# Kernel optimization log

Measured on AMD Instinct MI355X. Metric: run time of the kernel, lower is better.

Reference implementation:

```python
import jax, jax.numpy as jnp
import numpy as np

B, L, V, E, D, NH, HD, NL = 4, 2048, 32000, 300, 128, 4, 128, 3
D2 = NH * HD  # 512
W = 3  # ring window size (unfold_size)
EPS = 1e-5


def setup_inputs() -> dict:
    key = jax.random.key(0)
    ks = jax.random.split(key, 16)
    s = 0.02
    w = lambda k, shape: (jax.random.normal(k, shape, jnp.float32) * s)
    inp = {
        "tokens": jax.random.randint(ks[0], (B, L), 0, V),
        "mask": jax.random.randint(ks[1], (B, L), 0, 2).astype(jnp.int32),
        "emb_table": w(ks[2], (V, E)),
        "proj_w": w(ks[3], (D, E)),
        "proj_b": jnp.zeros((D,), jnp.float32),
        "ng": jnp.ones((NL, D), jnp.float32),
        "nb": jnp.zeros((NL, D), jnp.float32),
        "rq_w": w(ks[4], (NL, D2, D)), "rq_b": jnp.zeros((NL, D2), jnp.float32),
        "rk_w": w(ks[5], (NL, D2, D)), "rk_b": jnp.zeros((NL, D2), jnp.float32),
        "rv_w": w(ks[6], (NL, D2, D)), "rv_b": jnp.zeros((NL, D2), jnp.float32),
        "ro_w": w(ks[7], (NL, D, D2)), "ro_b": jnp.zeros((NL, D), jnp.float32),
        "sq_w": w(ks[8], (NL, D2, D)), "sq_b": jnp.zeros((NL, D2), jnp.float32),
        "sk_w": w(ks[9], (NL, D2, D)), "sk_b": jnp.zeros((NL, D2), jnp.float32),
        "sv_w": w(ks[10], (NL, D2, D)), "sv_b": jnp.zeros((NL, D2), jnp.float32),
        "so_w": w(ks[11], (NL, D, D2)), "so_b": jnp.zeros((NL, D), jnp.float32),
    }
    return inp


def _layernorm(x, g, b):
    mu = x.mean(-1, keepdims=True)
    var = x.var(-1, keepdims=True)
    return (x - mu) / jnp.sqrt(var + EPS) * g + b


def reference(tokens, mask, emb_table, proj_w, proj_b, ng, nb,
              rq_w, rq_b, rk_w, rk_b, rv_w, rv_b, ro_w, ro_b,
              sq_w, sq_b, sk_w, sk_b, sv_w, sv_b, so_w, so_b):
    b, l = tokens.shape
    pad = (mask == 0)                                        # [B,L] True at padding
    smask = jnp.concatenate([jnp.zeros((b, 1), bool), pad], axis=1)  # [B,L+1]
    x = emb_table[tokens] @ proj_w.T + proj_b                # [B,L,D]
    nodes = x
    relay = x.mean(axis=1)                                   # [B,D]
    r_embs = x                                               # fixed original embeddings
    scale = 1.0 / np.sqrt(HD).astype(np.float32)
    for i in range(NL):
        nx = _layernorm(nodes, ng[i], nb[i])
        # ----- MSA1: ring (windowed) attention + relay extras -----
        q = (nx @ rq_w[i].T + rq_b[i]).reshape(b, l, NH, HD)
        k = (nx @ rk_w[i].T + rk_b[i]).reshape(b, l, NH, HD)
        v = (nx @ rv_w[i].T + rv_b[i]).reshape(b, l, NH, HD)
        relay_bc = jnp.broadcast_to(relay[:, None, :], (b, l, D))
        ax = jnp.stack([r_embs, relay_bc], axis=2)           # [B,L,2,D]
        ak = (ax @ rk_w[i].T + rk_b[i]).reshape(b, l, 2, NH, HD)
        av = (ax @ rv_w[i].T + rv_b[i]).reshape(b, l, 2, NH, HD)
        kp = jnp.pad(k, ((0, 0), (1, 1), (0, 0), (0, 0)))    # zero pad like F.unfold
        vp = jnp.pad(v, ((0, 0), (1, 1), (0, 0), (0, 0)))
        kw = jnp.stack([kp[:, u:u + l] for u in range(W)], axis=2)  # [B,L,3,NH,HD]
        vw = jnp.stack([vp[:, u:u + l] for u in range(W)], axis=2)
        kall = jnp.concatenate([kw, ak], axis=2)             # [B,L,5,NH,HD]
        vall = jnp.concatenate([vw, av], axis=2)
        scores = jnp.einsum('blnh,blunh->blun', q, kall) * scale
        alphas = jax.nn.softmax(scores, axis=2)
        att = jnp.einsum('blun,blunh->blnh', alphas, vall).reshape(b, l, D2)
        nodes = nodes + jax.nn.leaky_relu(att @ ro_w[i].T + ro_b[i])
        # ----- MSA2: relay (global) attention over [relay; nodes] -----
        y = jnp.concatenate([relay[:, None, :], nodes], axis=1)      # [B,L+1,D]
        sq = (relay @ sq_w[i].T + sq_b[i]).reshape(b, NH, HD)
        sk = (y @ sk_w[i].T + sk_b[i]).reshape(b, l + 1, NH, HD)
        sv = (y @ sv_w[i].T + sv_b[i]).reshape(b, l + 1, NH, HD)
        pre = jnp.einsum('bnh,blnh->bnl', sq, sk) * scale            # [B,NH,L+1]
        pre = jnp.where(smask[:, None, :], -jnp.inf, pre)
        al = jax.nn.softmax(pre, axis=2)
        satt = jnp.einsum('bnl,blnh->bnh', al, sv).reshape(b, D2)
        relay = jax.nn.leaky_relu(satt @ so_w[i].T + so_b[i])
        nodes = jnp.where(pad[:, :, None], 0.0, nodes)
    return relay  # a_v: [B, d_model] (use_attention=False path)
```

## Files before the change

kernel.cpp:

```cpp
#include <hip/hip_runtime.h>
#include <hip/hip_bf16.h>

constexpr int B = 4, L = 2048, E = 300, D = 128, NH = 4, HD = 128, NL = 3, D2 = 512;
constexpr float EPS = 1e-5f;
constexpr float SCALE = 0.08838834764831843f;
constexpr int NCH = 64;

typedef unsigned int uint_t;
typedef unsigned short u16;
typedef short bf16x8 __attribute__((ext_vector_type(8)));
typedef float f32x4 __attribute__((ext_vector_type(4)));

__device__ __forceinline__ u16 f2bf(float f) {
  union { float f; uint_t i; } x; x.f = f;
  uint_t r = x.i + 0x7fffu + ((x.i >> 16) & 1u);
  return (u16)(r >> 16);
}
__device__ __forceinline__ uint_t packbf(float a, float b) {
  return (uint_t)f2bf(a) | ((uint_t)f2bf(b) << 16);
}
__device__ __forceinline__ float bf2f(u16 u) {
  union { uint_t i; float f; } x; x.i = ((uint_t)u) << 16; return x.f;
}
__device__ __forceinline__ float2 bf2x2(uint_t u) {
  union { uint_t i; float f; } a, b;
  a.i = (u & 0xffffu) << 16; b.i = u & 0xffff0000u;
  return make_float2(a.f, b.f);
}
struct f8 { float v[8]; };
__device__ __forceinline__ f8 unpack8(uint4 u) {
  f8 r;
  float2 a = bf2x2(u.x); r.v[0] = a.x; r.v[1] = a.y;
  float2 b = bf2x2(u.y); r.v[2] = b.x; r.v[3] = b.y;
  float2 c = bf2x2(u.z); r.v[4] = c.x; r.v[5] = c.y;
  float2 d = bf2x2(u.w); r.v[6] = d.x; r.v[7] = d.y;
  return r;
}

struct WCArgs { const float* s[4]; u16* d[4]; };
__global__ __launch_bounds__(256) void wconv(WCArgs wa) {
  int ti = blockIdx.y;
  const float* s = wa.s[ti]; u16* dd = wa.d[ti];
  int i = (blockIdx.x * 256 + threadIdx.x) * 4;
  float4 f = *(const float4*)(s + i);
  *(uint2*)(dd + i) = make_uint2(packbf(f.x, f.y), packbf(f.z, f.w));
}

struct GDesc { const u16* A; const u16* W; const float* bias; u16* outb; };
struct GArgs { GDesc d[5]; };
struct PArgs {
  const float* rel;
  const float* rkw; const float* rkb;
  const float* rvw; const float* rvb;
  const float* sqw; const float* sqb;
  const float* skw; const float* skb;
  float* relay_k; float* relay_v;
  float* u; float* cvec;
};
constexpr int NPROJ = 24;

__global__ __launch_bounds__(256) void gemm_qkv(GArgs ga, PArgs pa, int N) {
  int bid = blockIdx.x;
  int t = threadIdx.x;
  if (bid < NPROJ) {
    __shared__ float rel[D];
    __shared__ float sql2[2][HD];
    __shared__ float credp[4];
    int b = bid / 6, j = bid % 6;
    if (t < D) rel[t] = pa.rel[(size_t)b * D + t];
    __syncthreads();
    const float4* r4 = (const float4*)rel;
    if (j < 4) {
      int which = j >> 1;
      int n = (j & 1) * 256 + t;
      const float* W = which ? pa.rvw : pa.rkw;
      float acc = (which ? pa.rvb : pa.rkb)[n];
      const float4* w4 = (const float4*)(W + (size_t)n * D);
#pragma unroll 8
      for (int i = 0; i < D / 4; i++) {
        float4 w = w4[i], r = r4[i];
        acc += w.x * r.x + w.y * r.y + w.z * r.z + w.w * r.w;
      }
      (which ? pa.relay_v : pa.relay_k)[(size_t)b * D2 + n] = acc;
    } else {
      int hh = t >> 7, th = t & 127;
      int n = (j - 4) * 2 + hh;
      int nh = n * HD + th;
      float acc = pa.sqb[nh];
      const float4* w4 = (const float4*)(pa.sqw + (size_t)nh * D);
#pragma unroll 8
      for (int i = 0; i < D / 4; i++) {
        float4 w = w4[i], r = r4[i];
        acc += w.x * r.x + w.y * r.y + w.z * r.z + w.w * r.w;
      }
      sql2[hh][th] = acc;
      __syncthreads();
      float cp = acc * pa.skb[nh];
#pragma unroll
      for (int o = 1; o < 64; o <<= 1) cp += __shfl_xor(cp, o, 64);
      if ((t & 63) == 0) credp[t >> 6] = cp;
      float a0 = 0.f, a1 = 0.f, a2 = 0.f, a3 = 0.f;
      const float* wp = pa.skw + (size_t)(n * HD) * D + th;
      for (int hx = 0; hx < HD; hx += 4) {
        a0 += sql2[hh][hx] * wp[(size_t)hx * D];
        a1 += sql2[hh][hx + 1] * wp[(size_t)(hx + 1) * D];
        a2 += sql2[hh][hx + 2] * wp[(size_t)(hx + 2) * D];
        a3 += sql2[hh][hx + 3] * wp[(size_t)(hx + 3) * D];
      }
      pa.u[((size_t)b * NH + n) * D + th] = (a0 + a1 + a2 + a3) * SCALE;
      __syncthreads();
      if (th == 0) pa.cvec[b * NH + n] = (credp[2 * hh] + credp[2 * hh + 1]) * SCALE;
    }
    return;
  }
  __shared__ u16 As[128][136];
  __shared__ u16 Ws[128][136];
  int g = bid - NPROJ;
  int bm = g & 63;
  int y = g >> 6;
  int di = y >> 2, bn = y & 3;
  GDesc d = ga.d[di];
  const int rowA = bm * 128, rowW = bn * 128;

  f32x4 acc[4][4];
#pragma unroll
  for (int i = 0; i < 4; i++)
#pragma unroll
    for (int j = 0; j < 4; j++)
      acc[i][j] = (f32x4){0.f, 0.f, 0.f, 0.f};

  const int r = t >> 1, c0 = (t & 1) * 64;
  const int wid = t >> 6;
  const int wm = (wid & 1) * 64, wn = (wid >> 1) * 64;
  const int lr = t & 15, quad = (t >> 4) & 3;

  const u16* Arow = d.A + (size_t)(rowA + r) * 128;
  const u16* Wrow = d.W + (size_t)(rowW + r) * 128;
  uint4 av_[8], wv_[8];
#pragma unroll
  for (int i = 0; i < 8; i++) {
    av_[i] = *(const uint4*)(Arow + c0 + i * 8);
    wv_[i] = *(const uint4*)(Wrow + c0 + i * 8);
  }
#pragma unroll
  for (int i = 0; i < 8; i++) {
    *(uint4*)&As[r][c0 + i * 8] = av_[i];
    *(uint4*)&Ws[r][c0 + i * 8] = wv_[i];
  }
  __syncthreads();
#pragma unroll
  for (int ks = 0; ks < 4; ks++) {
    bf16x8 af[4], bfr[4];
#pragma unroll
    for (int mt = 0; mt < 4; mt++)
      af[mt] = *(const bf16x8*)&As[wm + mt * 16 + lr][ks * 32 + quad * 8];
#pragma unroll
    for (int nt = 0; nt < 4; nt++)
      bfr[nt] = *(const bf16x8*)&Ws[wn + nt * 16 + lr][ks * 32 + quad * 8];
#pragma unroll
    for (int mt = 0; mt < 4; mt++)
#pragma unroll
      for (int nt = 0; nt < 4; nt++)
        acc[mt][nt] = __builtin_amdgcn_mfma_f32_16x16x32_bf16(af[mt], bfr[nt], acc[mt][nt], 0, 0, 0);
  }
  __syncthreads();
#pragma unroll
  for (int nt = 0; nt < 4; nt++) {
    int colL = wn + nt * 16 + lr;
    float bv = d.bias[rowW + colL];
#pragma unroll
    for (int mt = 0; mt < 4; mt++) {
#pragma unroll
      for (int rr = 0; rr < 4; rr++) {
        int rowL = wm + mt * 16 + quad * 4 + rr;
        As[rowL][colL] = f2bf(acc[mt][nt][rr] + bv);
      }
    }
  }
  __syncthreads();
#pragma unroll
  for (int rep = 0; rep < 8; rep++) {
    int lin = rep * 256 + t;
    int rowL = lin >> 4, colL = (lin & 15) * 8;
    uint4 v = *(const uint4*)&As[rowL][colL];
    *(uint4*)&d.outb[(size_t)(rowA + rowL) * N + rowW + colL] = v;
  }
}

__global__ __launch_bounds__(256) void gemm_embed_ln(
    const float* __restrict__ emb, const float* __restrict__ W,
    const float* __restrict__ bias, const int* __restrict__ gather,
    const float* __restrict__ lng, const float* __restrict__ lnb,
    float* __restrict__ nodes, u16* __restrict__ xb, u16* __restrict__ nxb,
    float* __restrict__ relay) {
  __shared__ u16 As[64][72];
  __shared__ u16 Ws[128][72];
  __shared__ float C[64][132];
  __shared__ float gb[2][D];
  __shared__ float lmu[64], lrs[64];
  int t = threadIdx.x;
  int bm = blockIdx.x;
  const int rowA0 = bm * 64;

  f32x4 acc[2][4];
#pragma unroll
  for (int i = 0; i < 2; i++)
#pragma unroll
    for (int j = 0; j < 4; j++)
      acc[i][j] = (f32x4){0.f, 0.f, 0.f, 0.f};

  const int wid = t >> 6;
  const int wm = (wid & 1) * 32, wn = (wid >> 1) * 64;
  const int lr = t & 15, quad = (t >> 4) & 3;
  const int ra = t >> 2, ca = (t & 3) * 16;
  const int rw = t >> 1, cw = (t & 1) * 32;

  if (t < D) { gb[0][t] = lng[t]; gb[1][t] = lnb[t]; }

  const float* Arow = emb + (size_t)gather[rowA0 + ra] * E;
  const float* Wrow = W + (size_t)rw * E;

  for (int kt = 0; kt < E; kt += 64) {
    __syncthreads();
    bool full = (kt + 64 <= E);
#pragma unroll
    for (int ch = 0; ch < 4; ch++) {
      int c = kt + ca + ch * 4;
      float4 fa;
      if (full) fa = *(const float4*)(Arow + c);
      else {
        fa.x = (c + 0 < E) ? Arow[c + 0] : 0.f;
        fa.y = (c + 1 < E) ? Arow[c + 1] : 0.f;
        fa.z = (c + 2 < E) ? Arow[c + 2] : 0.f;
        fa.w = (c + 3 < E) ? Arow[c + 3] : 0.f;
      }
      *(uint2*)&As[ra][ca + ch * 4] = make_uint2(packbf(fa.x, fa.y), packbf(fa.z, fa.w));
    }
#pragma unroll
    for (int ch = 0; ch < 8; ch++) {
      int c = kt + cw + ch * 4;
      float4 fw;
      if (full) fw = *(const float4*)(Wrow + c);
      else {
        fw.x = (c + 0 < E) ? Wrow[c + 0] : 0.f;
        fw.y = (c + 1 < E) ? Wrow[c + 1] : 0.f;
        fw.z = (c + 2 < E) ? Wrow[c + 2] : 0.f;
        fw.w = (c + 3 < E) ? Wrow[c + 3] : 0.f;
      }
      *(uint2*)&Ws[rw][cw + ch * 4] = make_uint2(packbf(fw.x, fw.y), packbf(fw.z, fw.w));
    }
    __syncthreads();
#pragma unroll
    for (int ks = 0; ks < 2; ks++) {
      bf16x8 af[2], bfr[4];
#pragma unroll
      for (int mt = 0; mt < 2; mt++)
        af[mt] = *(const bf16x8*)&As[wm + mt * 16 + lr][ks * 32 + quad * 8];
#pragma unroll
      for (int nt = 0; nt < 4; nt++)
        bfr[nt] = *(const bf16x8*)&Ws[wn + nt * 16 + lr][ks * 32 + quad * 8];
#pragma unroll
      for (int mt = 0; mt < 2; mt++)
#pragma unroll
        for (int nt = 0; nt < 4; nt++)
          acc[mt][nt] = __builtin_amdgcn_mfma_f32_16x16x32_bf16(af[mt], bfr[nt], acc[mt][nt], 0, 0, 0);
    }
  }
#pragma unroll
  for (int nt = 0; nt < 4; nt++) {
    int col = wn + nt * 16 + lr;
    float bv = bias[col];
#pragma unroll
    for (int mt = 0; mt < 2; mt++) {
#pragma unroll
      for (int rr = 0; rr < 4; rr++) {
        int row = wm + mt * 16 + quad * 4 + rr;
        C[row][col] = acc[mt][nt][rr] + bv;
      }
    }
  }
  __syncthreads();
  if (t < 64) {
    float s = 0.f, s2 = 0.f;
#pragma unroll 16
    for (int j = 0; j < D; j++) { float v = C[t][j]; s += v; s2 += v * v; }
    float mu = s * (1.0f / D);
    float var = s2 * (1.0f / D) - mu * mu;
    lmu[t] = mu; lrs[t] = rsqrtf(var + EPS);
  }
  __syncthreads();
#pragma unroll
  for (int rep = 0; rep < 8; rep++) {
    int lin = rep * 1024 + t * 4;
    int row = lin >> 7, col = lin & 127;
    float4 v = *(const float4*)&C[row][col];
    size_t g = (size_t)(rowA0 + row) * D + col;
    *(float4*)&nodes[g] = v;
    *(uint2*)&xb[g] = make_uint2(packbf(v.x, v.y), packbf(v.z, v.w));
    float mu = lmu[row], rs = lrs[row];
    float o0 = (v.x - mu) * rs * gb[0][col] + gb[1][col];
    float o1 = (v.y - mu) * rs * gb[0][col + 1] + gb[1][col + 1];
    float o2 = (v.z - mu) * rs * gb[0][col + 2] + gb[1][col + 2];
    float o3 = (v.w - mu) * rs * gb[0][col + 3] + gb[1][col + 3];
    *(uint2*)&nxb[g] = make_uint2(packbf(o0, o1), packbf(o2, o3));
  }
  if (t < D) {
    int b = rowA0 >> 11;
    float s = 0.f;
#pragma unroll 16
    for (int r2 = 0; r2 < 64; r2++) s += C[r2][t];
    atomicAdd(&relay[b * D + t], s * (1.0f / L));
  }
}

__global__ __launch_bounds__(256) void gemm_ro_ln(
    const u16* __restrict__ A,
    const u16* __restrict__ W,
    const float* __restrict__ bias,
    const int* __restrict__ mask,
    const float* __restrict__ lng, const float* __restrict__ lnb,
    const float* __restrict__ uvec, const float* __restrict__ cvec,
    float* __restrict__ nodes, u16* __restrict__ nxb,
    float* __restrict__ pm, float* __restrict__ ps, float* __restrict__ pw,
    int do_ln) {
  __shared__ u16 As[32][136];
  __shared__ u16 Ws[128][136];
  __shared__ float C[32][132];
  __shared__ float gb[2][D];
  __shared__ float lmu[32], lrs[32];
  __shared__ float usv[NH][D];
  __shared__ float cv2[NH];
  __shared__ float scs[NH][32];
  __shared__ float esr[NH][32];
  int t = threadIdx.x;
  int bm = blockIdx.x;
  const int rowA0 = bm * 32;
  const int b4 = rowA0 >> 11;
  const int chunk = (rowA0 >> 5) & 63;

  f32x4 acc[4];
#pragma unroll
  for (int j = 0; j < 4; j++) acc[j] = (f32x4){0.f, 0.f, 0.f, 0.f};

  const int wid = t >> 6;
  const int wm = (wid & 1) * 16, wn = (wid >> 1) * 64;
  const int lr = t & 15, quad = (t >> 4) & 3;
  const int ra = t >> 3, ca = (t & 7) * 16;
  const int rw = t >> 1, cw = (t & 1) * 64;

  if (do_ln && t < D) { gb[0][t] = lng[t]; gb[1][t] = lnb[t]; }
#pragma unroll
  for (int rep = 0; rep < 2; rep++) {
    int idx = rep * 256 + t;
    usv[idx >> 7][idx & 127] = uvec[(size_t)b4 * NH * D + idx];
  }
  if (t < NH) cv2[t] = cvec[b4 * NH + t];

  const u16* Arow = A + (size_t)(rowA0 + ra) * 512;
  const u16* Wrow = W + (size_t)rw * 512;

  for (int kt = 0; kt < 512; kt += 128) {
    uint4 a0 = *(const uint4*)(Arow + kt + ca);
    uint4 a1 = *(const uint4*)(Arow + kt + ca + 8);
    uint4 w0 = *(const uint4*)(Wrow + kt + cw);
    uint4 w1 = *(const uint4*)(Wrow + kt + cw + 8);
    uint4 w2 = *(const uint4*)(Wrow + kt + cw + 16);
    uint4 w3 = *(const uint4*)(Wrow + kt + cw + 24);
    uint4 w4 = *(const uint4*)(Wrow + kt + cw + 32);
    uint4 w5 = *(const uint4*)(Wrow + kt + cw + 40);
    uint4 w6 = *(const uint4*)(Wrow + kt + cw + 48);
    uint4 w7 = *(const uint4*)(Wrow + kt + cw + 56);
    __syncthreads();
    *(uint4*)&As[ra][ca] = a0; *(uint4*)&As[ra][ca + 8] = a1;
    *(uint4*)&Ws[rw][cw] = w0; *(uint4*)&Ws[rw][cw + 8] = w1;
    *(uint4*)&Ws[rw][cw + 16] = w2; *(uint4*)&Ws[rw][cw + 24] = w3;
    *(uint4*)&Ws[rw][cw + 32] = w4; *(uint4*)&Ws[rw][cw + 40] = w5;
    *(uint4*)&Ws[rw][cw + 48] = w6; *(uint4*)&Ws[rw][cw + 56] = w7;
    __syncthreads();
#pragma unroll
    for (int ks = 0; ks < 4; ks++) {
      bf16x8 af = *(const bf16x8*)&As[wm + lr][ks * 32 + quad * 8];
      bf16x8 bfr[4];
#pragma unroll
      for (int nt = 0; nt < 4; nt++)
        bfr[nt] = *(const bf16x8*)&Ws[wn + nt * 16 + lr][ks * 32 + quad * 8];
#pragma unroll
      for (int nt = 0; nt < 4; nt++)
        acc[nt] = __builtin_amdgcn_mfma_f32_16x16x32_bf16(af, bfr[nt], acc[nt], 0, 0, 0);
    }
  }
  __syncthreads();
#pragma unroll
  for (int nt = 0; nt < 4; nt++) {
    int col = wn + nt * 16 + lr;
    float bv = bias[col];
#pragma unroll
    for (int rr = 0; rr < 4; rr++) {
      int row = wm + quad * 4 + rr;
      float v = acc[nt][rr] + bv;
      v = (v > 0.f) ? v : 0.01f * v;
      v += nodes[(size_t)(rowA0 + row) * D + col];
      if (mask[rowA0 + row] == 0) v = 0.f;
      C[row][col] = v;
    }
  }
  __syncthreads();
  if (t < 32) {
    float s = 0.f, s2 = 0.f;
#pragma unroll 16
    for (int j = 0; j < D; j++) { float v = C[t][j]; s += v; s2 += v * v; }
    float mu = s * (1.0f / D);
    float var = s2 * (1.0f / D) - mu * mu;
    lmu[t] = mu; lrs[t] = rsqrtf(var + EPS);
  }
  __syncthreads();
#pragma unroll
  for (int rep = 0; rep < 4; rep++) {
    int lin = rep * 1024 + t * 4;
    int row = lin >> 7, col = lin & 127;
    float4 v = *(const float4*)&C[row][col];
    size_t g = (size_t)(rowA0 + row) * D + col;
    *(float4*)&nodes[g] = v;
    if (do_ln) {
      float mu = lmu[row], rs = lrs[row];
      float o0 = (v.x - mu) * rs * gb[0][col] + gb[1][col];
      float o1 = (v.y - mu) * rs * gb[0][col + 1] + gb[1][col + 1];
      float o2 = (v.z - mu) * rs * gb[0][col + 2] + gb[1][col + 2];
      float o3 = (v.w - mu) * rs * gb[0][col + 3] + gb[1][col + 3];
      *(uint2*)&nxb[g] = make_uint2(packbf(o0, o1), packbf(o2, o3));
    }
  }
  {
    int n = wid, lane = t & 63;
    int bn = b4 * NH + n;
    const float2* un = (const float2*)usv[n];
    float2 uv2 = un[lane];
    for (int r2 = 0; r2 < 32; r2++) {
      float2 cc = ((const float2*)&C[r2][0])[lane];
      float p = uv2.x * cc.x + uv2.y * cc.y;
#pragma unroll
      for (int o = 1; o < 64; o <<= 1) p += __shfl_xor(p, o, 64);
      if (lane == 0) {
        float s = p + cv2[n];
        if (mask[rowA0 + r2] == 0) s = -1e30f;
        scs[n][r2] = s;
      }
    }
    float m = -1e30f;
    for (int r2 = 0; r2 < 32; r2++) m = fmaxf(m, scs[n][r2]);
    if (lane < 32) esr[n][lane] = expf(scs[n][lane] - m);
    float sum = 0.f;
    for (int r2 = 0; r2 < 32; r2++) sum += esr[n][r2];
    if (lane == 0) { pm[bn * NCH + chunk] = m; ps[bn * NCH + chunk] = sum; }
    float a0 = 0.f, a1 = 0.f;
    for (int r2 = 0; r2 < 32; r2++) {
      float e = esr[n][r2];
      float2 cc = ((const float2*)&C[r2][0])[lane];
      a0 += e * cc.x; a1 += e * cc.y;
    }
    float* pwp = pw + ((size_t)bn * NCH + chunk) * D + 2 * lane;
    pwp[0] = a0; pwp[1] = a1;
  }
}

__global__ __launch_bounds__(256) void ring_attn_kernel(
    const u16* __restrict__ q, const u16* __restrict__ k, const u16* __restrict__ v,
    const u16* __restrict__ akr, const u16* __restrict__ avr,
    const float* __restrict__ rk, const float* __restrict__ rv,
    u16* __restrict__ att) {
  int wv = threadIdx.x >> 6, lane = threadIdx.x & 63;
  int bl = blockIdx.x * 4 + wv;
  int b = bl >> 11, l = bl & (L - 1);
  size_t rowoff = (size_t)bl * D2 + lane * 8;

  uint4 qd = *(const uint4*)(q + rowoff);
  uint4 kd[5], vd[5];
  bool valid[3];
#pragma unroll
  for (int u = 0; u < 3; u++) {
    int ll = l + u - 1;
    valid[u] = (ll >= 0 && ll < L);
    size_t off = ((size_t)b * L + ll) * D2 + lane * 8;
    if (valid[u]) { kd[u] = *(const uint4*)(k + off); vd[u] = *(const uint4*)(v + off); }
    else { kd[u] = make_uint4(0, 0, 0, 0); vd[u] = make_uint4(0, 0, 0, 0); }
  }
  kd[3] = *(const uint4*)(akr + rowoff);
  vd[3] = *(const uint4*)(avr + rowoff);
  size_t rb = (size_t)b * D2 + lane * 8;
  float4 rk0 = *(const float4*)(rk + rb), rk1 = *(const float4*)(rk + rb + 4);
  float4 rv0 = *(const float4*)(rv + rb), rv1 = *(const float4*)(rv + rb + 4);

  f8 qf = unpack8(qd);
  f8 kf[5], vf[5];
#pragma unroll
  for (int u = 0; u < 4; u++) { kf[u] = unpack8(kd[u]); vf[u] = unpack8(vd[u]); }
  kf[4].v[0] = rk0.x; kf[4].v[1] = rk0.y; kf[4].v[2] = rk0.z; kf[4].v[3] = rk0.w;
  kf[4].v[4] = rk1.x; kf[4].v[5] = rk1.y; kf[4].v[6] = rk1.z; kf[4].v[7] = rk1.w;
  vf[4].v[0] = rv0.x; vf[4].v[1] = rv0.y; vf[4].v[2] = rv0.z; vf[4].v[3] = rv0.w;
  vf[4].v[4] = rv1.x; vf[4].v[5] = rv1.y; vf[4].v[6] = rv1.z; vf[4].v[7] = rv1.w;

  float s[5];
#pragma unroll
  for (int u = 0; u < 5; u++) {
    float p = 0.f;
#pragma unroll
    for (int j = 0; j < 8; j++) p += qf.v[j] * kf[u].v[j];
#pragma unroll
    for (int o = 1; o < 16; o <<= 1) p += __shfl_xor(p, o, 64);
    s[u] = p * SCALE;
  }
  float m = s[0];
#pragma unroll
  for (int u = 1; u < 5; u++) m = fmaxf(m, s[u]);
  float e[5], sum = 0.f;
#pragma unroll
  for (int u = 0; u < 5; u++) { e[u] = expf(s[u] - m); sum += e[u]; }
  float inv = 1.0f / sum;
  float o[8];
#pragma unroll
  for (int j = 0; j < 8; j++) {
    float a = 0.f;
#pragma unroll
    for (int u = 0; u < 5; u++) a += e[u] * vf[u].v[j];
    o[j] = a * inv;
  }
  uint4 od;
  od.x = packbf(o[0], o[1]); od.y = packbf(o[2], o[3]);
  od.z = packbf(o[4], o[5]); od.w = packbf(o[6], o[7]);
  *(uint4*)(att + rowoff) = od;
}

__global__ __launch_bounds__(512) void relay_combine(
    const float* __restrict__ pm, const float* __restrict__ ps,
    const float* __restrict__ pw,
    const float* __restrict__ relay_entry,
    const float* __restrict__ uvec_in, const float* __restrict__ cvec_in,
    const float* __restrict__ svw, const float* __restrict__ svb,
    const float* __restrict__ sow, const float* __restrict__ sob,
    float* __restrict__ relay_out) {
  __shared__ float rel0[D];
  __shared__ float wpart[8];
  __shared__ float ecs[NH][NCH];
  __shared__ float wsum[NH][D];
  __shared__ float satts[D2];
  __shared__ float rred[4][D];
  int b = blockIdx.x, t = threadIdx.x;
  int n = t >> 7, h = t & 127;
  int w = t >> 6, lane = t & 63;
  if (t < D) rel0[t] = relay_entry[(size_t)b * D + t];
  __syncthreads();
  float p = uvec_in[((size_t)b * NH + n) * D + h] * rel0[h];
#pragma unroll
  for (int o = 1; o < 64; o <<= 1) p += __shfl_xor(p, o, 64);
  if (lane == 0) wpart[w] = p;
  __syncthreads();
  float s0 = wpart[2 * n] + wpart[2 * n + 1] + cvec_in[b * NH + n];
  int c = h & 63;
  float pmv = pm[(b * NH + n) * NCH + c];
  float m = fmaxf(pmv, s0);
#pragma unroll
  for (int o = 1; o < 64; o <<= 1) m = fmaxf(m, __shfl_xor(m, o, 64));
  float ec = expf(pmv - m);
  if (h < 64) ecs[n][h] = ec;
  float sc = ps[(b * NH + n) * NCH + c] * ec;
#pragma unroll
  for (int o = 1; o < 64; o <<= 1) sc += __shfl_xor(sc, o, 64);
  float e0 = expf(s0 - m);
  float invS = 1.0f / (e0 + sc);
  __syncthreads();
  float acc = e0 * rel0[h];
  const float* pwp = pw + ((size_t)(b * NH + n) * NCH) * D + h;
#pragma unroll 8
  for (int cc = 0; cc < NCH; cc++) acc += ecs[n][cc] * pwp[(size_t)cc * D];
  wsum[n][h] = acc * invS;
  __syncthreads();
  {
    float a = svb[t];
    const float4* wp = (const float4*)(svw + (size_t)t * D);
    const float4* wl = (const float4*)wsum[n];
#pragma unroll 8
    for (int dd = 0; dd < D / 4; dd++) {
      float4 x = wl[dd], y = wp[dd];
      a += x.x * y.x + x.y * y.y + x.z * y.z + x.w * y.w;
    }
    satts[t] = a;
  }
  __syncthreads();
  {
    int part = t >> 7, col = t & 127;
    float a = 0.f;
    const float4* wp = (const float4*)(sow + (size_t)col * D2 + part * 128);
    const float4* a4 = (const float4*)(satts + part * 128);
#pragma unroll 8
    for (int jj = 0; jj < 32; jj++) {
      float4 x = a4[jj], y = wp[jj];
      a += x.x * y.x + x.y * y.y + x.z * y.z + x.w * y.w;
    }
    rred[part][col] = a;
  }
  __syncthreads();
  if (t < D) {
    float a = sob[t] + rred[0][t] + rred[1][t] + rred[2][t] + rred[3][t];
    a = (a > 0.f) ? a : 0.01f * a;
    relay_out[(size_t)b * D + t] = a;
  }
}

extern "C" void kernel_launch(void* const* d_in, const int* in_sizes, int n_in,
                              void* d_out, int out_size, void* d_ws, size_t ws_size,
                              hipStream_t stream) {
  const int* tokens = (const int*)d_in[0];
  const int* mask = (const int*)d_in[1];
  const float* emb = (const float*)d_in[2];
  const float* proj_w = (const float*)d_in[3];
  const float* proj_b = (const float*)d_in[4];
  const float* ng = (const float*)d_in[5];
  const float* nb = (const float*)d_in[6];
  const float* rq_w = (const float*)d_in[7], * rq_b = (const float*)d_in[8];
  const float* rk_w = (const float*)d_in[9], * rk_b = (const float*)d_in[10];
  const float* rv_w = (const float*)d_in[11], * rv_b = (const float*)d_in[12];
  const float* ro_w = (const float*)d_in[13], * ro_b = (const float*)d_in[14];
  const float* sq_w = (const float*)d_in[15], * sq_b = (const float*)d_in[16];
  const float* sk_w = (const float*)d_in[17], * sk_b = (const float*)d_in[18];
  const float* sv_w = (const float*)d_in[19], * sv_b = (const float*)d_in[20];
  const float* so_w = (const float*)d_in[21], * so_b = (const float*)d_in[22];

  const size_t BLD = (size_t)B * L * D;
  const size_t BLD4 = (size_t)B * L * D2;
  const size_t WTEN = (size_t)NL * D * D2;

  float* fp = (float*)d_ws;
  float* nodes = fp;                    fp += BLD;
  float* rbuf0 = fp;                    fp += B * D;
  float* rbuf1 = fp;                    fp += B * D;
  float* relay_k = fp;                  fp += B * D2;
  float* relay_v = fp;                  fp += B * D2;
  float* uv = fp;                       fp += B * NH * D;
  float* cv = fp;                       fp += B * NH;
  float* pm = fp;                       fp += B * NH * NCH;
  float* ps = fp;                       fp += B * NH * NCH;
  float* pw = fp;                       fp += (size_t)B * NH * NCH * D;
  u16* up = (u16*)fp;
  u16* xb = up;                         up += BLD;
  u16* nxb = up;                        up += BLD;
  u16* qb = up;                         up += BLD4;
  u16* kb = up;                         up += BLD4;
  u16* vb = up;                         up += BLD4;
  u16* akb = up;                        up += BLD4;
  u16* avb = up;                        up += BLD4;
  u16* attb = up;                       up += BLD4;
  u16* wb = up;
  u16* wrq = wb, * wrk = wb + WTEN, * wrv = wb + 2 * WTEN, * wro = wb + 3 * WTEN;

  hipMemsetAsync(rbuf0, 0, B * D * sizeof(float), stream);

  {
    WCArgs wa;
    wa.s[0] = rq_w; wa.s[1] = rk_w; wa.s[2] = rv_w; wa.s[3] = ro_w;
    wa.d[0] = wrq; wa.d[1] = wrk; wa.d[2] = wrv; wa.d[3] = wro;
    wconv<<<dim3(WTEN / 1024, 4), 256, 0, stream>>>(wa);
  }
  gemm_embed_ln<<<128, 256, 0, stream>>>(emb, proj_w, proj_b, tokens, ng, nb,
                                         nodes, xb, nxb, rbuf0);

  float* rin[3] = {rbuf0, rbuf1, rbuf0};
  float* rout[3] = {rbuf1, rbuf0, (float*)d_out};

  for (int i = 0; i < NL; i++) {
    const size_t wo = (size_t)i * D * D2;
    const float* rqbi = rq_b + (size_t)i * D2;
    const float* rkbi = rk_b + (size_t)i * D2;
    const float* rvbi = rv_b + (size_t)i * D2;
    const float* robi = ro_b + (size_t)i * D;
    const float* svwi = sv_w + wo, * svbi = sv_b + (size_t)i * D2;
    const float* sowi = so_w + wo, * sobi = so_b + (size_t)i * D;
    const int last = (i == NL - 1);

    {
      GArgs ga = {};
      ga.d[0] = {nxb, wrq + wo, rqbi, qb};
      ga.d[1] = {nxb, wrk + wo, rkbi, kb};
      ga.d[2] = {nxb, wrv + wo, rvbi, vb};
      ga.d[3] = {xb,  wrk + wo, rkbi, akb};
      ga.d[4] = {xb,  wrv + wo, rvbi, avb};
      PArgs pa;
      pa.rel = rin[i];
      pa.rkw = rk_w + wo; pa.rkb = rkbi;
      pa.rvw = rv_w + wo; pa.rvb = rvbi;
      pa.sqw = sq_w + wo; pa.sqb = sq_b + (size_t)i * D2;
      pa.skw = sk_w + wo; pa.skb = sk_b + (size_t)i * D2;
      pa.relay_k = relay_k; pa.relay_v = relay_v; pa.u = uv; pa.cvec = cv;
      gemm_qkv<<<64 * 20 + NPROJ, 256, 0, stream>>>(ga, pa, D2);
    }
    ring_attn_kernel<<<B * L / 4, 256, 0, stream>>>(qb, kb, vb, akb, avb, relay_k, relay_v, attb);
    gemm_ro_ln<<<256, 256, 0, stream>>>(
        attb, wro + wo, robi, mask,
        last ? nullptr : ng + (i + 1) * D, last ? nullptr : nb + (i + 1) * D,
        uv, cv, nodes, nxb, pm, ps, pw, last ? 0 : 1);
    relay_combine<<<B, 512, 0, stream>>>(pm, ps, pw, rin[i], uv, cv,
                                         svwi, svbi, sowi, sobi, rout[i]);
  }
}
```

Baseline: 361.4 us.

## Fuse ring attention into the output-projection/LayerNorm kernel

The separate ring-attention kernel is removed, and its per-row windowed softmax attention is computed inside the output-projection kernel. The result is written to shared memory instead of a global bf16 buffer. This removes one launch per layer and the global write and re-read of the attention tensor. In exchange, the attention work now runs on 256 blocks of 512 threads rather than 2048 small blocks, which lowers parallelism and latency hiding for a memory-bound stage. The GEMM tile per wave is also narrowed to match the larger block.

```diff
diff --git a/kernel.cpp b/kernel.cpp
--- a/kernel.cpp
+++ b/kernel.cpp
@@ -18,9 +18,6 @@
 }
 __device__ __forceinline__ uint_t packbf(float a, float b) {
   return (uint_t)f2bf(a) | ((uint_t)f2bf(b) << 16);
-}
-__device__ __forceinline__ float bf2f(u16 u) {
-  union { uint_t i; float f; } x; x.i = ((uint_t)u) << 16; return x.f;
 }
 __device__ __forceinline__ float2 bf2x2(uint_t u) {
   union { uint_t i; float f; } a, b;
@@ -313,8 +310,10 @@
   }
 }
 
-__global__ __launch_bounds__(256) void gemm_ro_ln(
-    const u16* __restrict__ A,
+__global__ __launch_bounds__(512) void attn_ro_ln(
+    const u16* __restrict__ q, const u16* __restrict__ k, const u16* __restrict__ v,
+    const u16* __restrict__ akr, const u16* __restrict__ avr,
+    const float* __restrict__ rkvec, const float* __restrict__ rvvec,
     const u16* __restrict__ W,
     const float* __restrict__ bias,
     const int* __restrict__ mask,
@@ -323,7 +322,7 @@
     float* __restrict__ nodes, u16* __restrict__ nxb,
     float* __restrict__ pm, float* __restrict__ ps, float* __restrict__ pw,
     int do_ln) {
-  __shared__ u16 As[32][136];
+  __shared__ u16 att[32][520];
   __shared__ u16 Ws[128][136];
   __shared__ float C[32][132];
   __shared__ float gb[2][D];
@@ -337,101 +336,146 @@
   const int rowA0 = bm * 32;
   const int b4 = rowA0 >> 11;
   const int chunk = (rowA0 >> 5) & 63;
-
-  f32x4 acc[4];
-#pragma unroll
-  for (int j = 0; j < 4; j++) acc[j] = (f32x4){0.f, 0.f, 0.f, 0.f};
-
-  const int wid = t >> 6;
-  const int wm = (wid & 1) * 16, wn = (wid >> 1) * 64;
+  const int wid = t >> 6, lane = t & 63;
+
+  if (do_ln && t < D) { gb[0][t] = lng[t]; gb[1][t] = lnb[t]; }
+  usv[t >> 7][t & 127] = uvec[(size_t)b4 * NH * D + t];
+  if (t < NH) cv2[t] = cvec[b4 * NH + t];
+
+  {
+    size_t rb = (size_t)b4 * D2 + lane * 8;
+    float4 rk0 = *(const float4*)(rkvec + rb), rk1 = *(const float4*)(rkvec + rb + 4);
+    float4 rv0 = *(const float4*)(rvvec + rb), rv1 = *(const float4*)(rvvec + rb + 4);
+    f8 krel, vrel;
+    krel.v[0] = rk0.x; krel.v[1] = rk0.y; krel.v[2] = rk0.z; krel.v[3] = rk0.w;
+    krel.v[4] = rk1.x; krel.v[5] = rk1.y; krel.v[6] = rk1.z; krel.v[7] = rk1.w;
+    vrel.v[0] = rv0.x; vrel.v[1] = rv0.y; vrel.v[2] = rv0.z; vrel.v[3] = rv0.w;
+    vrel.v[4] = rv1.x; vrel.v[5] = rv1.y; vrel.v[6] = rv1.z; vrel.v[7] = rv1.w;
+#pragma unroll
+    for (int i = 0; i < 4; i++) {
+      int rr_ = wid * 4 + i;
+      int gr = rowA0 + rr_;
+      int l = gr & (L - 1);
+      size_t rowoff = (size_t)gr * D2 + lane * 8;
+      uint4 qd = *(const uint4*)(q + rowoff);
+      uint4 kd[4], vd[4];
+#pragma unroll
+      for (int u2 = 0; u2 < 3; u2++) {
+        int ll = l + u2 - 1;
+        bool ok = (ll >= 0 && ll < L);
+        size_t off = rowoff + (size_t)(u2 - 1) * (size_t)D2;
+        if (ok) { kd[u2] = *(const uint4*)(k + off); vd[u2] = *(const uint4*)(v + off); }
+        else { kd[u2] = make_uint4(0, 0, 0, 0); vd[u2] = make_uint4(0, 0, 0, 0); }
+      }
+      kd[3] = *(const uint4*)(akr + rowoff);
+      vd[3] = *(const uint4*)(avr + rowoff);
+      f8 qf = unpack8(qd);
+      f8 kf[5], vf[5];
+#pragma unroll
+      for (int u2 = 0; u2 < 4; u2++) { kf[u2] = unpack8(kd[u2]); vf[u2] = unpack8(vd[u2]); }
+      kf[4] = krel; vf[4] = vrel;
+      float s[5];
+#pragma unroll
+      for (int u2 = 0; u2 < 5; u2++) {
+        float p = 0.f;
+#pragma unroll
+        for (int j = 0; j < 8; j++) p += qf.v[j] * kf[u2].v[j];
+#pragma unroll
+        for (int o = 1; o < 16; o <<= 1) p += __shfl_xor(p, o, 64);
+        s[u2] = p * SCALE;
+      }
+      float m = s[0];
+#pragma unroll
+      for (int u2 = 1; u2 < 5; u2++) m = fmaxf(m, s[u2]);
+      float e[5], sum = 0.f;
+#pragma unroll
+      for (int u2 = 0; u2 < 5; u2++) { e[u2] = expf(s[u2] - m); sum += e[u2]; }
+      float inv = 1.0f / sum;
+      float o8[8];
+#pragma unroll
+      for (int j = 0; j < 8; j++) {
+        float a = 0.f;
+#pragma unroll
+        for (int u2 = 0; u2 < 5; u2++) a += e[u2] * vf[u2].v[j];
+        o8[j] = a * inv;
+      }
+      uint4 od;
+      od.x = packbf(o8[0], o8[1]); od.y = packbf(o8[2], o8[3]);
+      od.z = packbf(o8[4], o8[5]); od.w = packbf(o8[6], o8[7]);
+      *(uint4*)&att[rr_][lane * 8] = od;
+    }
+  }
+  __syncthreads();
+
+  f32x4 acc[2];
+  acc[0] = (f32x4){0.f, 0.f, 0.f, 0.f};
+  acc[1] = (f32x4){0.f, 0.f, 0.f, 0.f};
+  const int wm = (wid & 1) * 16, wn = (wid >> 1) * 32;
   const int lr = t & 15, quad = (t >> 4) & 3;
-  const int ra = t >> 3, ca = (t & 7) * 16;
-  const int rw = t >> 1, cw = (t & 1) * 64;
-
-  if (do_ln && t < D) { gb[0][t] = lng[t]; gb[1][t] = lnb[t]; }
-#pragma unroll
-  for (int rep = 0; rep < 2; rep++) {
-    int idx = rep * 256 + t;
-    usv[idx >> 7][idx & 127] = uvec[(size_t)b4 * NH * D + idx];
-  }
-  if (t < NH) cv2[t] = cvec[b4 * NH + t];
-
-  const u16* Arow = A + (size_t)(rowA0 + ra) * 512;
+  const int rw = t >> 2, cw = (t & 3) * 32;
   const u16* Wrow = W + (size_t)rw * 512;
-
   for (int kt = 0; kt < 512; kt += 128) {
-    uint4 a0 = *(const uint4*)(Arow + kt + ca);
-    uint4 a1 = *(const uint4*)(Arow + kt + ca + 8);
     uint4 w0 = *(const uint4*)(Wrow + kt + cw);
     uint4 w1 = *(const uint4*)(Wrow + kt + cw + 8);
     uint4 w2 = *(const uint4*)(Wrow + kt + cw + 16);
     uint4 w3 = *(const uint4*)(Wrow + kt + cw + 24);
-    uint4 w4 = *(const uint4*)(Wrow + kt + cw + 32);
-    uint4 w5 = *(const uint4*)(Wrow + kt + cw + 40);
-    uint4 w6 = *(const uint4*)(Wrow + kt + cw + 48);
-    uint4 w7 = *(const uint4*)(Wrow + kt + cw + 56);
     __syncthreads();
-    *(uint4*)&As[ra][ca] = a0; *(uint4*)&As[ra][ca + 8] = a1;
     *(uint4*)&Ws[rw][cw] = w0; *(uint4*)&Ws[rw][cw + 8] = w1;
     *(uint4*)&Ws[rw][cw + 16] = w2; *(uint4*)&Ws[rw][cw + 24] = w3;
-    *(uint4*)&Ws[rw][cw + 32] = w4; *(uint4*)&Ws[rw][cw + 40] = w5;
-    *(uint4*)&Ws[rw][cw + 48] = w6; *(uint4*)&Ws[rw][cw + 56] = w7;
     __syncthreads();
 #pragma unroll
     for (int ks = 0; ks < 4; ks++) {
-      bf16x8 af = *(const bf16x8*)&As[wm + lr][ks * 32 + quad * 8];
-      bf16x8 bfr[4];
-#pragma unroll
-      for (int nt = 0; nt < 4; nt++)
-        bfr[nt] = *(const bf16x8*)&Ws[wn + nt * 16 + lr][ks * 32 + quad * 8];
-#pragma unroll
-      for (int nt = 0; nt < 4; nt++)
-        acc[nt] = __builtin_amdgcn_mfma_f32_16x16x32_bf16(af, bfr[nt], acc[nt], 0, 0, 0);
-    }
-  }
-  __syncthreads();
-#pragma unroll
-  for (int nt = 0; nt < 4; nt++) {
+      bf16x8 af = *(const bf16x8*)&att[wm + lr][kt + ks * 32 + quad * 8];
+#pragma unroll
+      for (int nt = 0; nt < 2; nt++) {
+        bf16x8 bfr = *(const bf16x8*)&Ws[wn + nt * 16 + lr][ks * 32 + quad * 8];
+        acc[nt] = __builtin_amdgcn_mfma_f32_16x16x32_bf16(af, bfr, acc[nt], 0, 0, 0);
+      }
+    }
+  }
+  __syncthreads();
+#pragma unroll
+  for (int nt = 0; nt < 2; nt++) {
     int col = wn + nt * 16 + lr;
     float bv = bias[col];
 #pragma unroll
     for (int rr = 0; rr < 4; rr++) {
       int row = wm + quad * 4 + rr;
-      float v = acc[nt][rr] + bv;
-      v = (v > 0.f) ? v : 0.01f * v;
-      v += nodes[(size_t)(rowA0 + row) * D + col];
-      if (mask[rowA0 + row] == 0) v = 0.f;
-      C[row][col] = v;
+      float vv = acc[nt][rr] + bv;
+      vv = (vv > 0.f) ? vv : 0.01f * vv;
+      vv += nodes[(size_t)(rowA0 + row) * D + col];
+      if (mask[rowA0 + row] == 0) vv = 0.f;
+      C[row][col] = vv;
     }
   }
   __syncthreads();
   if (t < 32) {
     float s = 0.f, s2 = 0.f;
 #pragma unroll 16
-    for (int j = 0; j < D; j++) { float v = C[t][j]; s += v; s2 += v * v; }
+    for (int j = 0; j < D; j++) { float vv = C[t][j]; s += vv; s2 += vv * vv; }
     float mu = s * (1.0f / D);
     float var = s2 * (1.0f / D) - mu * mu;
     lmu[t] = mu; lrs[t] = rsqrtf(var + EPS);
   }
   __syncthreads();
 #pragma unroll
-  for (int rep = 0; rep < 4; rep++) {
-    int lin = rep * 1024 + t * 4;
+  for (int rep = 0; rep < 2; rep++) {
+    int lin = rep * 2048 + t * 4;
     int row = lin >> 7, col = lin & 127;
-    float4 v = *(const float4*)&C[row][col];
+    float4 vv = *(const float4*)&C[row][col];
     size_t g = (size_t)(rowA0 + row) * D + col;
-    *(float4*)&nodes[g] = v;
+    *(float4*)&nodes[g] = vv;
     if (do_ln) {
       float mu = lmu[row], rs = lrs[row];
-      float o0 = (v.x - mu) * rs * gb[0][col] + gb[1][col];
-      float o1 = (v.y - mu) * rs * gb[0][col + 1] + gb[1][col + 1];
-      float o2 = (v.z - mu) * rs * gb[0][col + 2] + gb[1][col + 2];
-      float o3 = (v.w - mu) * rs * gb[0][col + 3] + gb[1][col + 3];
+      float o0 = (vv.x - mu) * rs * gb[0][col] + gb[1][col];
+      float o1 = (vv.y - mu) * rs * gb[0][col + 1] + gb[1][col + 1];
+      float o2 = (vv.z - mu) * rs * gb[0][col + 2] + gb[1][col + 2];
+      float o3 = (vv.w - mu) * rs * gb[0][col + 3] + gb[1][col + 3];
       *(uint2*)&nxb[g] = make_uint2(packbf(o0, o1), packbf(o2, o3));
     }
   }
-  {
-    int n = wid, lane = t & 63;
+  if (wid < 4) {
+    int n = wid;
     int bn = b4 * NH + n;
     const float2* un = (const float2*)usv[n];
     float2 uv2 = un[lane];
@@ -461,73 +505,6 @@
     float* pwp = pw + ((size_t)bn * NCH + chunk) * D + 2 * lane;
     pwp[0] = a0; pwp[1] = a1;
   }
-}
-
-__global__ __launch_bounds__(256) void ring_attn_kernel(
-    const u16* __restrict__ q, const u16* __restrict__ k, const u16* __restrict__ v,
-    const u16* __restrict__ akr, const u16* __restrict__ avr,
-    const float* __restrict__ rk, const float* __restrict__ rv,
-    u16* __restrict__ att) {
-  int wv = threadIdx.x >> 6, lane = threadIdx.x & 63;
-  int bl = blockIdx.x * 4 + wv;
-  int b = bl >> 11, l = bl & (L - 1);
-  size_t rowoff = (size_t)bl * D2 + lane * 8;
-
-  uint4 qd = *(const uint4*)(q + rowoff);
-  uint4 kd[5], vd[5];
-  bool valid[3];
-#pragma unroll
-  for (int u = 0; u < 3; u++) {
-    int ll = l + u - 1;
-    valid[u] = (ll >= 0 && ll < L);
-    size_t off = ((size_t)b * L + ll) * D2 + lane * 8;
-    if (valid[u]) { kd[u] = *(const uint4*)(k + off); vd[u] = *(const uint4*)(v + off); }
-    else { kd[u] = make_uint4(0, 0, 0, 0); vd[u] = make_uint4(0, 0, 0, 0); }
-  }
-  kd[3] = *(const uint4*)(akr + rowoff);
-  vd[3] = *(const uint4*)(avr + rowoff);
-  size_t rb = (size_t)b * D2 + lane * 8;
-  float4 rk0 = *(const float4*)(rk + rb), rk1 = *(const float4*)(rk + rb + 4);
-  float4 rv0 = *(const float4*)(rv + rb), rv1 = *(const float4*)(rv + rb + 4);
-
-  f8 qf = unpack8(qd);
-  f8 kf[5], vf[5];
-#pragma unroll
-  for (int u = 0; u < 4; u++) { kf[u] = unpack8(kd[u]); vf[u] = unpack8(vd[u]); }
-  kf[4].v[0] = rk0.x; kf[4].v[1] = rk0.y; kf[4].v[2] = rk0.z; kf[4].v[3] = rk0.w;
-  kf[4].v[4] = rk1.x; kf[4].v[5] = rk1.y; kf[4].v[6] = rk1.z; kf[4].v[7] = rk1.w;
-  vf[4].v[0] = rv0.x; vf[4].v[1] = rv0.y; vf[4].v[2] = rv0.z; vf[4].v[3] = rv0.w;
-  vf[4].v[4] = rv1.x; vf[4].v[5] = rv1.y; vf[4].v[6] = rv1.z; vf[4].v[7] = rv1.w;
-
-  float s[5];
-#pragma unroll
-  for (int u = 0; u < 5; u++) {
-    float p = 0.f;
-#pragma unroll
-    for (int j = 0; j < 8; j++) p += qf.v[j] * kf[u].v[j];
-#pragma unroll
-    for (int o = 1; o < 16; o <<= 1) p += __shfl_xor(p, o, 64);
-    s[u] = p * SCALE;
-  }
-  float m = s[0];
-#pragma unroll
-  for (int u = 1; u < 5; u++) m = fmaxf(m, s[u]);
-  float e[5], sum = 0.f;
-#pragma unroll
-  for (int u = 0; u < 5; u++) { e[u] = expf(s[u] - m); sum += e[u]; }
-  float inv = 1.0f / sum;
-  float o[8];
-#pragma unroll
-  for (int j = 0; j < 8; j++) {
-    float a = 0.f;
-#pragma unroll
-    for (int u = 0; u < 5; u++) a += e[u] * vf[u].v[j];
-    o[j] = a * inv;
-  }
-  uint4 od;
-  od.x = packbf(o[0], o[1]); od.y = packbf(o[2], o[3]);
-  od.z = packbf(o[4], o[5]); od.w = packbf(o[6], o[7]);
-  *(uint4*)(att + rowoff) = od;
 }
 
 __global__ __launch_bounds__(512) void relay_combine(
@@ -648,7 +625,6 @@
   u16* vb = up;                         up += BLD4;
   u16* akb = up;                        up += BLD4;
   u16* avb = up;                        up += BLD4;
-  u16* attb = up;                       up += BLD4;
   u16* wb = up;
   u16* wrq = wb, * wrk = wb + WTEN, * wrv = wb + 2 * WTEN, * wro = wb + 3 * WTEN;
 
@@ -692,9 +668,9 @@
       pa.relay_k = relay_k; pa.relay_v = relay_v; pa.u = uv; pa.cvec = cv;
       gemm_qkv<<<64 * 20 + NPROJ, 256, 0, stream>>>(ga, pa, D2);
     }
-    ring_attn_kernel<<<B * L / 4, 256, 0, stream>>>(qb, kb, vb, akb, avb, relay_k, relay_v, attb);
-    gemm_ro_ln<<<256, 256, 0, stream>>>(
-        attb, wro + wo, robi, mask,
+    attn_ro_ln<<<256, 512, 0, stream>>>(
+        qb, kb, vb, akb, avb, relay_k, relay_v,
+        wro + wo, robi, mask,
         last ? nullptr : ng + (i + 1) * D, last ? nullptr : nb + (i + 1) * D,
         uv, cv, nodes, nxb, pm, ps, pw, last ? 0 : 1);
     relay_combine<<<B, 512, 0, stream>>>(pm, ps, pw, rin[i], uv, cv,
```

Result: faster. 340.4 us (-5.8%).
